# Optimization experiments

Hardware: AMD Instinct MI355X
Metric: run time of the kernel (lower is better)

The kernel has to match this reference:

```python
import jax, jax.numpy as jnp
import numpy as np

N = 50000
E = 800000
EPS = 1e-5


def gcn_conv(x, W, b, src, dst, n):
    # PyG GCNConv: h = xW; add self-loops; symmetric norm D^-1/2 A_hat D^-1/2; out = agg + bias
    h = x @ W                                            # [N, out]
    deg = jax.ops.segment_sum(jnp.ones_like(src, dtype=h.dtype), dst, num_segments=n) + 1.0
    inv_sqrt = jax.lax.rsqrt(deg)                        # [N]
    coef = inv_sqrt[src] * inv_sqrt[dst]                 # [E]
    agg = jax.ops.segment_sum(h[src] * coef[:, None], dst, num_segments=n)
    agg = agg + h * (inv_sqrt * inv_sqrt)[:, None]       # self-loop term
    return agg + b


def batchnorm(h, gamma, beta):
    mean = jnp.mean(h, axis=0)
    var = jnp.var(h, axis=0)
    return gamma * (h - mean) * jax.lax.rsqrt(var + EPS) + beta


def setup_inputs() -> dict:
    key = jax.random.key(0)
    ks = jax.random.split(key, 8)
    x = jax.random.normal(ks[0], (N, 128), dtype=jnp.float32)
    edge_index = jax.random.randint(ks[1], (2, E), 0, N, dtype=jnp.int64)
    s = 1.0 / np.sqrt(128)
    W1 = jax.random.uniform(ks[2], (128, 128), jnp.float32, -s, s)
    W2 = jax.random.uniform(ks[3], (128, 128), jnp.float32, -s, s)
    W3 = jax.random.uniform(ks[4], (128, 64), jnp.float32, -s, s)
    b1 = jnp.zeros((128,), jnp.float32)
    b2 = jnp.zeros((128,), jnp.float32)
    b3 = jnp.zeros((64,), jnp.float32)
    g1 = jnp.ones((128,), jnp.float32)
    bt1 = jnp.zeros((128,), jnp.float32)
    g2 = jnp.ones((128,), jnp.float32)
    bt2 = jnp.zeros((128,), jnp.float32)
    return {"x": x, "edge_index": edge_index, "W1": W1, "b1": b1, "g1": g1, "bt1": bt1,
            "W2": W2, "b2": b2, "g2": g2, "bt2": bt2, "W3": W3, "b3": b3}


def reference(x, edge_index, W1, b1, g1, bt1, W2, b2, g2, bt2, W3, b3):
    src, dst = edge_index[0], edge_index[1]
    h = gcn_conv(x, W1, b1, src, dst, N)
    h = jax.nn.relu(batchnorm(h, g1, bt1))
    h = gcn_conv(h, W2, b2, src, dst, N)
    h = jax.nn.relu(batchnorm(h, g2, bt2))
    out = gcn_conv(h, W3, b3, src, dst, N)
    return out
```

## Files before the change

### kernel.cpp

```cpp
#include <hip/hip_runtime.h>

#define N_NODES 50000
#define N_EDGES 800000
static constexpr float EPS = 1e-5f;
static constexpr int NCH   = 16;
static constexpr int EPC   = N_EDGES / NCH;
static constexpr int NW    = (N_NODES + 3) / 4;
static constexpr int SCAN_NB = (N_NODES + 1023) / 1024;
static constexpr int GEMM_NB = (N_NODES + 63) / 64;
static constexpr int FILL_NB = (N_EDGES + 1023) / 1024;
static constexpr int WCONV_NB = 160;

using bf16x8 = __attribute__((ext_vector_type(8))) short;
using f32x4  = __attribute__((ext_vector_type(4))) float;

static __device__ __forceinline__ unsigned short f2bf(float f) {
    unsigned int u = __float_as_uint(f);
    return (unsigned short)((u + 0x7FFFu + ((u >> 16) & 1u)) >> 16);
}
static __device__ __forceinline__ float blo(unsigned int w) { return __uint_as_float(w << 16); }
static __device__ __forceinline__ float bhi(unsigned int w) { return __uint_as_float(w & 0xffff0000u); }

__global__ __launch_bounds__(256) void k_hist_wconv(
    const int* __restrict__ ei, unsigned char* __restrict__ rank8,
    unsigned int* __restrict__ basesU,
    const float* __restrict__ W1, const float* __restrict__ W2,
    const float* __restrict__ W3,
    unsigned short* __restrict__ Wf1, unsigned short* __restrict__ Wf2,
    unsigned short* __restrict__ Wf3, int4* __restrict__ statz) {
    __shared__ unsigned int h[NW];
    const int t = threadIdx.x;
    if (blockIdx.x < NCH) {
        for (int i = t; i < NW; i += 256) h[i] = 0;
        __syncthreads();
        const int cbeg = blockIdx.x * EPC;
        for (int e0 = cbeg + t * 4; e0 < cbeg + EPC; e0 += 1024) {
            int4 d4 = *(const int4*)&ei[N_EDGES + e0];
            int sh0 = (d4.x & 3) * 8, sh1 = (d4.y & 3) * 8;
            int sh2 = (d4.z & 3) * 8, sh3 = (d4.w & 3) * 8;
            unsigned int o0 = atomicAdd(&h[d4.x >> 2], 1u << sh0);
            unsigned int o1 = atomicAdd(&h[d4.y >> 2], 1u << sh1);
            unsigned int o2 = atomicAdd(&h[d4.z >> 2], 1u << sh2);
            unsigned int o3 = atomicAdd(&h[d4.w >> 2], 1u << sh3);
            unsigned int pk = ((o0 >> sh0) & 0xffu) | (((o1 >> sh1) & 0xffu) << 8)
                            | (((o2 >> sh2) & 0xffu) << 16) | (((o3 >> sh3) & 0xffu) << 24);
            *(unsigned int*)&rank8[e0] = pk;
        }
        __syncthreads();
        for (int i = t; i < NW; i += 256)
            basesU[blockIdx.x * NW + i] = h[i];
    } else {
        int gid = (blockIdx.x - NCH) * 256 + t;
        if (gid < 128) statz[gid] = make_int4(0, 0, 0, 0);
        const float* W; unsigned short* Wf; int NCOL, idx;
        if (gid < 16384)      { W = W1; Wf = Wf1; NCOL = 128; idx = gid; }
        else if (gid < 32768) { W = W2; Wf = Wf2; NCOL = 128; idx = gid - 16384; }
        else                  { W = W3; Wf = Wf3; NCOL = 64;  idx = gid - 32768; }
        int j  = idx & 7;
        int l  = (idx >> 3) & 63;
        int s  = (idx >> 9) & 3;
        int tn = idx >> 11;
        int n = tn * 16 + (l & 15);
        int k = s * 32 + (l >> 4) * 8 + j;
        Wf[idx] = f2bf(W[k * NCOL + n]);
    }
}

template <int NCOL, bool BN, bool ABF16>
static __device__ __forceinline__ void gemm_body(
    int row0, int t,
    const void* __restrict__ Ap, const unsigned short* __restrict__ Wf,
    const float* __restrict__ stats,
    const float* __restrict__ gamma, const float* __restrict__ beta,
    unsigned short* __restrict__ H,
    unsigned short* As, float* sc_s, float* sh_s) {
    if (BN) {
        if (t < 128) {
            float s  = stats[t];
            float sq = stats[128 + t];
            float mean = s * (1.0f / N_NODES);
            float var  = sq * (1.0f / N_NODES) - mean * mean;
            float sc = gamma[t] * rsqrtf(var + EPS);
            sc_s[t] = sc;
            sh_s[t] = beta[t] - mean * sc;
        }
        __syncthreads();
    }

#pragma unroll
    for (int i = 0; i < 4; i++) {
        int q = i * 256 + t;
        int row = q >> 4;
        int c8  = (q & 15) * 8;
        int grow = row0 + row;
        float v[8];
        if (grow < N_NODES) {
            if (ABF16) {
                uint4 p = *(const uint4*)((const unsigned short*)Ap + (size_t)grow * 128 + c8);
                v[0] = blo(p.x); v[1] = bhi(p.x); v[2] = blo(p.y); v[3] = bhi(p.y);
                v[4] = blo(p.z); v[5] = bhi(p.z); v[6] = blo(p.w); v[7] = bhi(p.w);
            } else {
                const float* Af = (const float*)Ap + (size_t)grow * 128 + c8;
                float4 f0 = *(const float4*)Af;
                float4 f1 = *(const float4*)(Af + 4);
                v[0] = f0.x; v[1] = f0.y; v[2] = f0.z; v[3] = f0.w;
                v[4] = f1.x; v[5] = f1.y; v[6] = f1.z; v[7] = f1.w;
            }
        } else {
#pragma unroll
            for (int j = 0; j < 8; j++) v[j] = 0.f;
        }
        if (BN) {
#pragma unroll
            for (int j = 0; j < 8; j++)
                v[j] = fmaxf(fmaf(v[j], sc_s[c8 + j], sh_s[c8 + j]), 0.f);
        }
        uint4 pk;
        pk.x = (unsigned)f2bf(v[0]) | ((unsigned)f2bf(v[1]) << 16);
        pk.y = (unsigned)f2bf(v[2]) | ((unsigned)f2bf(v[3]) << 16);
        pk.z = (unsigned)f2bf(v[4]) | ((unsigned)f2bf(v[5]) << 16);
        pk.w = (unsigned)f2bf(v[6]) | ((unsigned)f2bf(v[7]) << 16);
        *(uint4*)&As[row * 136 + c8] = pk;
    }
    __syncthreads();

    const int wv = t >> 6;
    const int l  = t & 63;
    const int m  = l & 15;
    const int kq = l >> 4;

    bf16x8 afrag[4];
    const unsigned short* arow = &As[(wv * 16 + m) * 136 + kq * 8];
#pragma unroll
    for (int s = 0; s < 4; s++)
        afrag[s] = *(const bf16x8*)(arow + s * 32);

    constexpr int NT = NCOL / 16;
#pragma unroll
    for (int tn = 0; tn < NT; tn++) {
        f32x4 acc = {0.f, 0.f, 0.f, 0.f};
#pragma unroll
        for (int s = 0; s < 4; s++) {
            bf16x8 b = *(const bf16x8*)&Wf[(size_t)((tn * 4 + s) * 64 + l) * 8];
            acc = __builtin_amdgcn_mfma_f32_16x16x32_bf16(afrag[s], b, acc, 0, 0, 0);
        }
        int col = tn * 16 + m;
#pragma unroll
        for (int r = 0; r < 4; r++) {
            int row = row0 + wv * 16 + kq * 4 + r;
            if (row < N_NODES) H[(size_t)row * NCOL + col] = f2bf(acc[r]);
        }
    }
}

template <int NCOL>
__global__ __launch_bounds__(256) void k_gemm_bn(
    const unsigned short* __restrict__ A, const unsigned short* __restrict__ Wf,
    const float* __restrict__ stats,
    const float* __restrict__ gamma, const float* __restrict__ beta,
    unsigned short* __restrict__ H) {
    __shared__ unsigned short As[64 * 136];
    __shared__ float sc_s[128], sh_s[128];
    gemm_body<NCOL, true, true>(blockIdx.x * 64, threadIdx.x, A, Wf, stats,
                                gamma, beta, H, As, sc_s, sh_s);
}

__global__ __launch_bounds__(256) void k_gemm1_scan1(
    const float* __restrict__ x, const unsigned short* __restrict__ Wf1,
    unsigned short* __restrict__ h1,
    unsigned int* __restrict__ basesU, float* __restrict__ inv_sqrt,
    int* __restrict__ excl, int* __restrict__ partials) {
    __shared__ unsigned short As[64 * 136];
    __shared__ float sc_s[128], sh_s[128];
    const int t = threadIdx.x;
    if (blockIdx.x < GEMM_NB) {
        gemm_body<128, false, false>(blockIdx.x * 64, t, x, Wf1,
                                     nullptr, nullptr, nullptr, h1, As, sc_s, sh_s);
    } else {
        int* shi = (int*)As;
        const int g = (blockIdx.x - GEMM_NB) * 256 + t;
        int r0 = 0, r1 = 0, r2 = 0, r3 = 0;
        if (g < NW) {
#pragma unroll
            for (int c = 0; c < NCH; c++) {
                unsigned int w = basesU[c * NW + g];
                unsigned int pb = (unsigned)r0 | ((unsigned)r1 << 8)
                                | ((unsigned)r2 << 16) | ((unsigned)r3 << 24);
                basesU[c * NW + g] = pb;
                r0 += w & 0xff; r1 += (w >> 8) & 0xff;
                r2 += (w >> 16) & 0xff; r3 += (w >> 24) & 0xff;
            }
        }
        int S = r0 + r1 + r2 + r3;
        shi[t] = S;
        __syncthreads();
        for (int off = 1; off < 256; off <<= 1) {
            int u = (t >= off) ? shi[t - off] : 0;
            __syncthreads();
            shi[t] += u;
            __syncthreads();
        }
        int base = shi[t] - S;
        if (g < NW) {
            int i0 = g * 4;
            *(int4*)&excl[i0] = make_int4(base, base + r0, base + r0 + r1,
                                          base + r0 + r1 + r2);
            *(float4*)&inv_sqrt[i0] = make_float4(
                rsqrtf((float)r0 + 1.0f), rsqrtf((float)r1 + 1.0f),
                rsqrtf((float)r2 + 1.0f), rsqrtf((float)r3 + 1.0f));
        }
        if (t == 255) partials[blockIdx.x - GEMM_NB] = shi[t];
    }
}

__global__ __launch_bounds__(256) void k_scan2_fill(
    const int* __restrict__ excl, const int* __restrict__ partials,
    int* __restrict__ rowptr,
    const int* __restrict__ ei, const unsigned char* __restrict__ rank8,
    const unsigned char* __restrict__ cb8,
    int* __restrict__ esrc) {
    const int t = threadIdx.x;
    __shared__ int sh[256];
    __shared__ int ps[256];
    int v = (t < SCAN_NB) ? partials[t] : 0;
    sh[t] = v;
    __syncthreads();
    for (int off = 1; off < 256; off <<= 1) {
        int u = (t >= off) ? sh[t - off] : 0;
        __syncthreads();
        sh[t] += u;
        __syncthreads();
    }
    ps[t] = sh[t] - v;
    __syncthreads();

    if (blockIdx.x < SCAN_NB) {
        int i0 = (blockIdx.x * 256 + t) * 4;
        if (i0 < N_NODES) {
            int4 e4 = *(const int4*)&excl[i0];
            int b = ps[blockIdx.x];
            *(int4*)&rowptr[i0] = make_int4(e4.x + b, e4.y + b, e4.z + b, e4.w + b);
        }
        if (blockIdx.x == 0 && t == 0) rowptr[N_NODES] = N_EDGES;
    } else {
        int e0 = ((blockIdx.x - SCAN_NB) * 256 + t) * 4;
        if (e0 < N_EDGES) {
            const int c = e0 / EPC;
            const unsigned char* cb = cb8 + (size_t)c * N_NODES;
            int4 s4 = *(const int4*)&ei[e0];
            int4 d4 = *(const int4*)&ei[N_EDGES + e0];
            unsigned int r4 = *(const unsigned int*)&rank8[e0];
            int p0 = excl[d4.x] + ps[d4.x >> 10] + cb[d4.x] + (r4 & 0xff);
            int p1 = excl[d4.y] + ps[d4.y >> 10] + cb[d4.y] + ((r4 >> 8) & 0xff);
            int p2 = excl[d4.z] + ps[d4.z >> 10] + cb[d4.z] + ((r4 >> 16) & 0xff);
            int p3 = excl[d4.w] + ps[d4.w >> 10] + cb[d4.w] + ((r4 >> 24) & 0xff);
            esrc[p0] = s4.x;
            esrc[p1] = s4.y;
            esrc[p2] = s4.z;
            esrc[p3] = s4.w;
        }
    }
}

template <int F, bool OUTBF>
__global__ __launch_bounds__(256) void k_agg(const int* __restrict__ rowptr,
                                             const int* __restrict__ esrc,
                                             const float* __restrict__ inv_sqrt,
                                             const unsigned short* __restrict__ H,
                                             const float* __restrict__ bias,
                                             void* __restrict__ OUT) {
    constexpr int LPN = F / 8;
    constexpr int NPB = 256 / LPN;
    const int t = threadIdx.x;
    const int node = blockIdx.x * NPB + t / LPN;
    const int lane = t % LPN;
    if (node >= N_NODES) return;

    const uint4* __restrict__ Hv = (const uint4*)H;
    const int beg = rowptr[node];
    const int end = rowptr[node + 1];
    const float rsn = inv_sqrt[node];

    float acc[8];
#pragma unroll
    for (int i = 0; i < 8; i++) acc[i] = 0.f;

#define ACC8(P, C)                                                     \
    acc[0] = fmaf(blo((P).x), (C), acc[0]);                            \
    acc[1] = fmaf(bhi((P).x), (C), acc[1]);                            \
    acc[2] = fmaf(blo((P).y), (C), acc[2]);                            \
    acc[3] = fmaf(bhi((P).y), (C), acc[3]);                            \
    acc[4] = fmaf(blo((P).z), (C), acc[4]);                            \
    acc[5] = fmaf(bhi((P).z), (C), acc[5]);                            \
    acc[6] = fmaf(blo((P).w), (C), acc[6]);                            \
    acc[7] = fmaf(bhi((P).w), (C), acc[7]);

    int j = beg;
    for (; j + 7 < end; j += 8) {
        int4 sa = *(const int4*)&esrc[j];
        int4 sb = *(const int4*)&esrc[j + 4];
        uint4 p0 = Hv[(size_t)sa.x * LPN + lane];
        uint4 p1 = Hv[(size_t)sa.y * LPN + lane];
        uint4 p2 = Hv[(size_t)sa.z * LPN + lane];
        uint4 p3 = Hv[(size_t)sa.w * LPN + lane];
        uint4 p4 = Hv[(size_t)sb.x * LPN + lane];
        uint4 p5 = Hv[(size_t)sb.y * LPN + lane];
        uint4 p6 = Hv[(size_t)sb.z * LPN + lane];
        uint4 p7 = Hv[(size_t)sb.w * LPN + lane];
        float c0 = inv_sqrt[sa.x] * rsn, c1 = inv_sqrt[sa.y] * rsn;
        float c2 = inv_sqrt[sa.z] * rsn, c3 = inv_sqrt[sa.w] * rsn;
        float c4 = inv_sqrt[sb.x] * rsn, c5 = inv_sqrt[sb.y] * rsn;
        float c6 = inv_sqrt[sb.z] * rsn, c7 = inv_sqrt[sb.w] * rsn;
        ACC8(p0, c0) ACC8(p1, c1) ACC8(p2, c2) ACC8(p3, c3)
        ACC8(p4, c4) ACC8(p5, c5) ACC8(p6, c6) ACC8(p7, c7)
    }
    if (j + 3 < end) {
        int4 sa = *(const int4*)&esrc[j];
        uint4 p0 = Hv[(size_t)sa.x * LPN + lane];
        uint4 p1 = Hv[(size_t)sa.y * LPN + lane];
        uint4 p2 = Hv[(size_t)sa.z * LPN + lane];
        uint4 p3 = Hv[(size_t)sa.w * LPN + lane];
        float c0 = inv_sqrt[sa.x] * rsn, c1 = inv_sqrt[sa.y] * rsn;
        float c2 = inv_sqrt[sa.z] * rsn, c3 = inv_sqrt[sa.w] * rsn;
        ACC8(p0, c0) ACC8(p1, c1) ACC8(p2, c2) ACC8(p3, c3)
        j += 4;
    }
    for (; j < end; j++) {
        int s0 = esrc[j];
        float c0 = inv_sqrt[s0] * rsn;
        uint4 p0 = Hv[(size_t)s0 * LPN + lane];
        ACC8(p0, c0)
    }
#undef ACC8

    uint4 ps = Hv[(size_t)node * LPN + lane];
    float idv = rsn * rsn;
    float4 b0 = ((const float4*)bias)[lane * 2];
    float4 b1 = ((const float4*)bias)[lane * 2 + 1];
    acc[0] = fmaf(blo(ps.x), idv, acc[0]) + b0.x;
    acc[1] = fmaf(bhi(ps.x), idv, acc[1]) + b0.y;
    acc[2] = fmaf(blo(ps.y), idv, acc[2]) + b0.z;
    acc[3] = fmaf(bhi(ps.y), idv, acc[3]) + b0.w;
    acc[4] = fmaf(blo(ps.z), idv, acc[4]) + b1.x;
    acc[5] = fmaf(bhi(ps.z), idv, acc[5]) + b1.y;
    acc[6] = fmaf(blo(ps.w), idv, acc[6]) + b1.z;
    acc[7] = fmaf(bhi(ps.w), idv, acc[7]) + b1.w;

    if (OUTBF) {
        uint4 pk;
        pk.x = (unsigned)f2bf(acc[0]) | ((unsigned)f2bf(acc[1]) << 16);
        pk.y = (unsigned)f2bf(acc[2]) | ((unsigned)f2bf(acc[3]) << 16);
        pk.z = (unsigned)f2bf(acc[4]) | ((unsigned)f2bf(acc[5]) << 16);
        pk.w = (unsigned)f2bf(acc[6]) | ((unsigned)f2bf(acc[7]) << 16);
        ((uint4*)OUT)[(size_t)node * LPN + lane] = pk;
    } else {
        float4* o = (float4*)OUT + ((size_t)node * LPN + lane) * 2;
        o[0] = make_float4(acc[0], acc[1], acc[2], acc[3]);
        o[1] = make_float4(acc[4], acc[5], acc[6], acc[7]);
    }
}

__global__ __launch_bounds__(256) void k_stats(const unsigned short* __restrict__ A,
                                               float* __restrict__ stats) {
    const int t  = threadIdx.x;
    const int c4 = t & 31;
    const int rr = t >> 5;
    float4 sum = make_float4(0.f, 0.f, 0.f, 0.f);
    float4 sq  = make_float4(0.f, 0.f, 0.f, 0.f);
    for (int row = blockIdx.x * 8 + rr; row < N_NODES; row += gridDim.x * 8) {
        uint2 p = *(const uint2*)&A[(size_t)row * 128 + c4 * 4];
        float vx = blo(p.x), vy = bhi(p.x), vz = blo(p.y), vw = bhi(p.y);
        sum.x += vx; sum.y += vy; sum.z += vz; sum.w += vw;
        sq.x += vx * vx; sq.y += vy * vy; sq.z += vz * vz; sq.w += vw * vw;
    }
    __shared__ float4 red[2][8][32];
    red[0][rr][c4] = sum;
    red[1][rr][c4] = sq;
    __syncthreads();
    if (t < 32) {
        float4 s = make_float4(0.f, 0.f, 0.f, 0.f);
        float4 q = make_float4(0.f, 0.f, 0.f, 0.f);
#pragma unroll
        for (int i = 0; i < 8; i++) {
            float4 a = red[0][i][t];
            float4 b = red[1][i][t];
            s.x += a.x; s.y += a.y; s.z += a.z; s.w += a.w;
            q.x += b.x; q.y += b.y; q.z += b.z; q.w += b.w;
        }
        int c = t * 4;
        atomicAdd(&stats[c + 0], s.x); atomicAdd(&stats[c + 1], s.y);
        atomicAdd(&stats[c + 2], s.z); atomicAdd(&stats[c + 3], s.w);
        atomicAdd(&stats[128 + c + 0], q.x); atomicAdd(&stats[128 + c + 1], q.y);
        atomicAdd(&stats[128 + c + 2], q.z); atomicAdd(&stats[128 + c + 3], q.w);
    }
}

extern "C" void kernel_launch(void* const* d_in, const int* in_sizes, int n_in,
                              void* d_out, int out_size, void* d_ws, size_t ws_size,
                              hipStream_t stream) {
    const float* x   = (const float*)d_in[0];
    const int*   ei  = (const int*)d_in[1];
    const float* W1  = (const float*)d_in[2];
    const float* b1  = (const float*)d_in[3];
    const float* g1  = (const float*)d_in[4];
    const float* bt1 = (const float*)d_in[5];
    const float* W2  = (const float*)d_in[6];
    const float* b2  = (const float*)d_in[7];
    const float* g2  = (const float*)d_in[8];
    const float* bt2 = (const float*)d_in[9];
    const float* W3  = (const float*)d_in[10];
    const float* b3  = (const float*)d_in[11];
    float* out = (float*)d_out;

    char* ws = (char*)d_ws;
    size_t off = 0;
    auto alloc = [&](size_t bytes) { char* p = ws + off; off += (bytes + 255) & ~(size_t)255; return p; };
    float* stats1   = (float*)alloc(256 * 4);
    float* stats2   = (float*)alloc(256 * 4);
    unsigned int*  basesU = (unsigned int*)alloc((size_t)NCH * NW * 4);
    unsigned char* rank8  = (unsigned char*)alloc((size_t)N_EDGES);
    float* inv_sqrt = (float*)alloc((size_t)N_NODES * 4);
    int*   excl     = (int*)  alloc((size_t)N_NODES * 4);
    int*   partials = (int*)  alloc(256 * 4);
    int*   rowptr   = (int*)  alloc((size_t)(N_NODES + 1) * 4);
    int*   esrc     = (int*)  alloc((size_t)N_EDGES * 4);
    unsigned short* Wf1 = (unsigned short*)alloc((size_t)128 * 128 * 2);
    unsigned short* Wf2 = (unsigned short*)alloc((size_t)128 * 128 * 2);
    unsigned short* Wf3 = (unsigned short*)alloc((size_t)64 * 128 * 2);
    unsigned short* h1  = (unsigned short*)alloc((size_t)N_NODES * 128 * 2);
    unsigned short* h2  = (unsigned short*)alloc((size_t)N_NODES * 128 * 2);
    unsigned short* h3  = (unsigned short*)alloc((size_t)N_NODES * 64 * 2);
    unsigned short* agg1 = (unsigned short*)alloc((size_t)N_NODES * 128 * 2);
    unsigned short* agg2 = (unsigned short*)alloc((size_t)N_NODES * 128 * 2);

    k_hist_wconv<<<NCH + WCONV_NB, 256, 0, stream>>>(ei, rank8, basesU,
                                                     W1, W2, W3, Wf1, Wf2, Wf3,
                                                     (int4*)stats1);
    k_gemm1_scan1<<<GEMM_NB + SCAN_NB, 256, 0, stream>>>(x, Wf1, h1, basesU,
                                                         inv_sqrt, excl, partials);
    k_scan2_fill<<<SCAN_NB + FILL_NB, 256, 0, stream>>>(excl, partials, rowptr,
                                                        ei, rank8,
                                                        (const unsigned char*)basesU,
                                                        esrc);
    k_agg<128, true><<<N_NODES / 16, 256, 0, stream>>>(rowptr, esrc, inv_sqrt, h1, b1, agg1);
    k_stats<<<256, 256, 0, stream>>>(agg1, stats1);
    k_gemm_bn<128><<<GEMM_NB, 256, 0, stream>>>(agg1, Wf2, stats1, g1, bt1, h2);
    k_agg<128, true><<<N_NODES / 16, 256, 0, stream>>>(rowptr, esrc, inv_sqrt, h2, b2, agg2);
    k_stats<<<256, 256, 0, stream>>>(agg2, stats2);
    k_gemm_bn<64><<<GEMM_NB, 256, 0, stream>>>(agg2, Wf3, stats2, g2, bt2, h3);
    k_agg<64, false><<<(N_NODES + 31) / 32, 256, 0, stream>>>(rowptr, esrc, inv_sqrt, h3, b3, out);
}
```

Before: 306.5 us.

## Double GEMM row tile to 128 and stage bf16 output through LDS for coalesced stores

The dense transform GEMM now processes 128 rows per block instead of 64, so each wave computes two 16-row MFMA tiles and reuses each loaded weight fragment for both. The results are written back into the shared tile and then copied out as 16-byte row-contiguous stores instead of scattered 2-byte stores. This cuts weight-fragment reloads and improves store coalescing, at the cost of twice the LDS, extra barriers, fewer blocks and more registers per thread.

```diff
diff --git a/kernel.cpp b/kernel.cpp
--- a/kernel.cpp
+++ b/kernel.cpp
@@ -7,7 +7,7 @@
 static constexpr int EPC   = N_EDGES / NCH;
 static constexpr int NW    = (N_NODES + 3) / 4;
 static constexpr int SCAN_NB = (N_NODES + 1023) / 1024;
-static constexpr int GEMM_NB = (N_NODES + 63) / 64;
+static constexpr int GEMM_NB = (N_NODES + 127) / 128;
 static constexpr int FILL_NB = (N_EDGES + 1023) / 1024;
 static constexpr int WCONV_NB = 160;
 
@@ -88,7 +88,7 @@
     }
 
 #pragma unroll
-    for (int i = 0; i < 4; i++) {
+    for (int i = 0; i < 8; i++) {
         int q = i * 256 + t;
         int row = q >> 4;
         int c8  = (q & 15) * 8;
@@ -129,28 +129,50 @@
     const int m  = l & 15;
     const int kq = l >> 4;
 
-    bf16x8 afrag[4];
-    const unsigned short* arow = &As[(wv * 16 + m) * 136 + kq * 8];
-#pragma unroll
-    for (int s = 0; s < 4; s++)
-        afrag[s] = *(const bf16x8*)(arow + s * 32);
+    bf16x8 a0[4], a1[4];
+    const unsigned short* ar0 = &As[(wv * 32 + m) * 136 + kq * 8];
+    const unsigned short* ar1 = &As[(wv * 32 + 16 + m) * 136 + kq * 8];
+#pragma unroll
+    for (int s = 0; s < 4; s++) {
+        a0[s] = *(const bf16x8*)(ar0 + s * 32);
+        a1[s] = *(const bf16x8*)(ar1 + s * 32);
+    }
+    __syncthreads();
 
     constexpr int NT = NCOL / 16;
 #pragma unroll
     for (int tn = 0; tn < NT; tn++) {
-        f32x4 acc = {0.f, 0.f, 0.f, 0.f};
+        f32x4 c0 = {0.f, 0.f, 0.f, 0.f};
+        f32x4 c1 = {0.f, 0.f, 0.f, 0.f};
 #pragma unroll
         for (int s = 0; s < 4; s++) {
             bf16x8 b = *(const bf16x8*)&Wf[(size_t)((tn * 4 + s) * 64 + l) * 8];
-            acc = __builtin_amdgcn_mfma_f32_16x16x32_bf16(afrag[s], b, acc, 0, 0, 0);
+            c0 = __builtin_amdgcn_mfma_f32_16x16x32_bf16(a0[s], b, c0, 0, 0, 0);
+            c1 = __builtin_amdgcn_mfma_f32_16x16x32_bf16(a1[s], b, c1, 0, 0, 0);
         }
         int col = tn * 16 + m;
 #pragma unroll
         for (int r = 0; r < 4; r++) {
-            int row = row0 + wv * 16 + kq * 4 + r;
-            if (row < N_NODES) H[(size_t)row * NCOL + col] = f2bf(acc[r]);
-        }
-    }
+            As[(wv * 32 + kq * 4 + r) * 136 + col]      = f2bf(c0[r]);
+            As[(wv * 32 + 16 + kq * 4 + r) * 136 + col] = f2bf(c1[r]);
+        }
+    }
+    __syncthreads();
+
+    constexpr int GPR  = NCOL / 8;
+    constexpr int ITER = 128 * GPR / 256;
+#pragma unroll
+    for (int i = 0; i < ITER; i++) {
+        int q = i * 256 + t;
+        int row = q / GPR;
+        int c8  = (q % GPR) * 8;
+        int grow = row0 + row;
+        if (grow < N_NODES) {
+            uint4 pk = *(const uint4*)&As[row * 136 + c8];
+            *(uint4*)&H[(size_t)grow * NCOL + c8] = pk;
+        }
+    }
+    __syncthreads();
 }
 
 template <int NCOL>
@@ -159,9 +181,9 @@
     const float* __restrict__ stats,
     const float* __restrict__ gamma, const float* __restrict__ beta,
     unsigned short* __restrict__ H) {
-    __shared__ unsigned short As[64 * 136];
+    __shared__ unsigned short As[128 * 136];
     __shared__ float sc_s[128], sh_s[128];
-    gemm_body<NCOL, true, true>(blockIdx.x * 64, threadIdx.x, A, Wf, stats,
+    gemm_body<NCOL, true, true>(blockIdx.x * 128, threadIdx.x, A, Wf, stats,
                                 gamma, beta, H, As, sc_s, sh_s);
 }
 
@@ -170,11 +192,11 @@
     unsigned short* __restrict__ h1,
     unsigned int* __restrict__ basesU, float* __restrict__ inv_sqrt,
     int* __restrict__ excl, int* __restrict__ partials) {
-    __shared__ unsigned short As[64 * 136];
+    __shared__ unsigned short As[128 * 136];
     __shared__ float sc_s[128], sh_s[128];
     const int t = threadIdx.x;
     if (blockIdx.x < GEMM_NB) {
-        gemm_body<128, false, false>(blockIdx.x * 64, t, x, Wf1,
+        gemm_body<128, false, false>(blockIdx.x * 128, t, x, Wf1,
                                      nullptr, nullptr, nullptr, h1, As, sc_s, sh_s);
     } else {
         int* shi = (int*)As;
```

Measured after the change: 302.3 us. Within noise of the previous version (-1.4%).
